# Optimization experiments

Measured on AMD Instinct MI355X. Metric: run time of the kernel, lower is better.

## Reference

```python
import jax, jax.numpy as jnp
import numpy as np

ATTEN_DIM = 64

def setup_inputs() -> dict:
    key = jax.random.key(0)
    ks = jax.random.split(key, 7)
    b, c, h, w = 16, 2048, 32, 32
    d_att, d_emb = 64, 64
    x = jax.random.normal(ks[0], (b, c, h, w), dtype=jnp.float32)
    # 1x1 conv == per-position linear; store weights as [out, in]
    scale = 1.0 / np.sqrt(c)
    wq = jax.random.normal(ks[1], (d_att, c), dtype=jnp.float32) * scale
    wk = jax.random.normal(ks[2], (d_att, c), dtype=jnp.float32) * scale
    wv = jax.random.normal(ks[3], (d_emb, c), dtype=jnp.float32) * scale
    bq = jnp.zeros((d_att,), dtype=jnp.float32)
    bk = jnp.zeros((d_att,), dtype=jnp.float32)
    bv = jnp.zeros((d_emb,), dtype=jnp.float32)
    return {"x": x, "wq": wq, "bq": bq, "wk": wk, "bk": bk, "wv": wv, "bv": bv}


def reference(x, wq, bq, wk, bk, wv, bv):
    b, c, h, w = x.shape
    # 1x1 conv projections: [b,c,h,w] x [d,c] -> [b,d,h,w]
    q = jnp.einsum('bchw,dc->bdhw', x, wq) + bq[None, :, None, None]
    k = jnp.einsum('bchw,dc->bdhw', x, wk) + bk[None, :, None, None]
    v = jnp.einsum('bchw,dc->bdhw', x, wv) + bv[None, :, None, None]
    # full non-local attention scores [b, h, w, h, w]
    atten = jnp.einsum('bcxy,bcij->bxyij', q, k) / ATTEN_DIM  # NOTE: module divides by atten_dim, not sqrt
    atten = jax.nn.softmax(atten.reshape(b, h, w, h * w), axis=-1).reshape(b, h, w, h, w)
    out = jnp.einsum('bxyij,bdij->bxyd', atten, v)
    return jnp.transpose(out, (0, 3, 1, 2))  # [b, emb_dim, h, w]
```

## Files before the change

### kernel.cpp

```cpp
#include <hip/hip_runtime.h>

typedef float f32x4 __attribute__((ext_vector_type(4)));
typedef short s16x8 __attribute__((ext_vector_type(8)));
typedef unsigned u32x4 __attribute__((ext_vector_type(4)));
typedef unsigned short u16;
typedef unsigned short u16x8 __attribute__((ext_vector_type(8)));

__device__ __forceinline__ u16 f2bf(float f) {
  unsigned u = __builtin_bit_cast(unsigned, f);
  u += 0x7fffu + ((u >> 16) & 1u);
  return (u16)(u >> 16);
}

__device__ __forceinline__ unsigned cvt_pk_bf16(float a, float b) {
  unsigned r;
  asm("v_cvt_pk_bf16_f32 %0, %1, %2" : "=v"(r) : "v"(a), "v"(b));
  return r;
}

#define AS1 __attribute__((address_space(1)))
#define AS3 __attribute__((address_space(3)))
#define GLD16(g, l) __builtin_amdgcn_global_load_lds((const AS1 unsigned int*)(g), (AS3 unsigned int*)(l), 16, 0, 0)

#define CEXP 0.0225421101f

__global__ __launch_bounds__(256) void prepack_w(
    const float* __restrict__ wq, const float* __restrict__ wk, const float* __restrict__ wv,
    u16* __restrict__ Wpk)
{
  const int d = blockIdx.x;
  const int t = threadIdx.x;
  const int kc = t >> 3, blk = t & 7;
  const int key = (d >> 1) & 7;
  const float* src = (d < 64) ? (wq + (size_t)d * 2048)
                   : (d < 128) ? (wk + (size_t)(d - 64) * 2048)
                               : (wv + (size_t)(d - 128) * 2048);
  const float* s8 = src + kc * 64 + ((blk ^ key) << 3);
  u16x8 o;
#pragma unroll
  for (int j = 0; j < 8; ++j) o[j] = f2bf(s8[j]);
  *(u16x8*)(Wpk + ((size_t)(kc * 192 + d) << 6) + (blk << 3)) = o;
}

__global__ __launch_bounds__(512) void qkv_proj(
    const float* __restrict__ x, const u16* __restrict__ Wpk,
    const float* __restrict__ bq, const float* __restrict__ bk, const float* __restrict__ bv,
    u16* __restrict__ Qo, u16* __restrict__ Ko, u16* __restrict__ Vt)
{
  const int b   = blockIdx.x >> 4;
  const int p0  = (blockIdx.x & 15) * 64;
  const int tid = threadIdx.x;
  const int lane = tid & 63;
  const int wid  = tid >> 6;
  const int l15 = lane & 15, l4 = lane >> 4;
  const int wm = wid & 1, wn = wid >> 1;

  __shared__ __align__(16) u16 lA[4][64 * 64];
  __shared__ __align__(16) u16 lB[4][192 * 64];

  const int pg = lane & 15;
  const int kb = wid * 4 + (lane >> 4);
  const int k0 = kb * 4;
  const int ww = wid - 4;

  f32x4 acc[2][3];
#pragma unroll
  for (int m = 0; m < 2; ++m)
#pragma unroll
    for (int n = 0; n < 3; ++n) acc[m][n] = (f32x4)(0.0f);

  const float* xb = x + (size_t)b * 2048 * 1024 + p0 + pg * 4;
  float4 SA[8], SB[8];

  auto xload2 = [&](int c, float4 (&S)[8]) {
#pragma unroll
    for (int cc = 0; cc < 2; ++cc) {
      const float* g = xb + (size_t)((c + cc) * 64 + k0) * 1024;
#pragma unroll
      for (int r = 0; r < 4; ++r) S[cc * 4 + r] = *(const float4*)(g + r * 1024);
    }
  };
  auto xstore2 = [&](int c, float4 (&S)[8]) {
#pragma unroll
    for (int cc = 0; cc < 2; ++cc) {
      const int slot = (c + cc) & 3;
#pragma unroll
      for (int col = 0; col < 4; ++col) {
        int p = pg * 4 + col;
        unsigned lo = cvt_pk_bf16(S[cc * 4 + 0][col], S[cc * 4 + 1][col]);
        unsigned hi = cvt_pk_bf16(S[cc * 4 + 2][col], S[cc * 4 + 3][col]);
        int swz = ((kb >> 1) ^ ((p >> 1) & 7)) & 7;
        char* dst = (char*)&lA[0][0] + slot * 8192 + p * 128 + (swz << 4) + (kb & 1) * 8;
        *(uint2*)dst = make_uint2(lo, hi);
      }
    }
  };
  auto wissue2 = [&](int c) {
#pragma unroll
    for (int cc = 0; cc < 2; ++cc) {
      const int slot = (c + cc) & 3;
      const u16* g = Wpk + (size_t)(c + cc) * 12288 + lane * 8;
#pragma unroll
      for (int j = 0; j < 6; ++j) {
        int q = ww * 6 + j;
        GLD16(g + q * 512, &lB[0][0] + slot * 12288 + q * 512);
      }
    }
  };
  auto domfma = [&](int slot) {
#pragma unroll
    for (int ks = 0; ks < 2; ++ks) {
      s16x8 af[2], bfv[3];
#pragma unroll
      for (int m = 0; m < 2; ++m) {
        int p = wm * 32 + m * 16 + l15;
        int swz = ((ks * 4 + l4) ^ ((p >> 1) & 7)) & 7;
        af[m] = *(const s16x8*)((const char*)&lA[0][0] + slot * 8192 + p * 128 + (swz << 4));
      }
#pragma unroll
      for (int n = 0; n < 3; ++n) {
        int d = wn * 48 + n * 16 + l15;
        int swz = ((ks * 4 + l4) ^ ((d >> 1) & 7)) & 7;
        bfv[n] = *(const s16x8*)((const char*)&lB[0][0] + slot * 24576 + d * 128 + (swz << 4));
      }
#pragma unroll
      for (int m = 0; m < 2; ++m)
#pragma unroll
        for (int n = 0; n < 3; ++n)
          acc[m][n] = __builtin_amdgcn_mfma_f32_16x16x32_bf16(af[m], bfv[n], acc[m][n], 0, 0, 0);
    }
  };
  auto barrier = [&]() {
    if (wid < 4) asm volatile("s_waitcnt lgkmcnt(0)" ::: "memory");
    else         asm volatile("s_waitcnt vmcnt(0) lgkmcnt(0)" ::: "memory");
    __builtin_amdgcn_sched_barrier(0);
    __builtin_amdgcn_s_barrier();
    __builtin_amdgcn_sched_barrier(0);
  };
  auto step = [&](int t, float4 (&Sl)[8], float4 (&Ss)[8]) {
    if (wid < 4) { if (t < 14) xload2(2 * t + 4, Sl); }
    else         { if (t < 15) wissue2(2 * t + 2); }
    __builtin_amdgcn_s_setprio(1);
    domfma((2 * t) & 3);
    domfma((2 * t + 1) & 3);
    __builtin_amdgcn_s_setprio(0);
    if (wid < 4 && t < 15) xstore2(2 * t + 2, Ss);
    barrier();
  };

  if (wid < 4) { xload2(0, SA); xload2(2, SB); xstore2(0, SA); }
  else         { wissue2(0); }
  barrier();

  for (int tt = 0; tt < 8; ++tt) {
    step(2 * tt,     SA, SB);
    step(2 * tt + 1, SB, SA);
  }

#pragma unroll
  for (int n = 0; n < 3; ++n) {
    const int dg = wn * 48 + n * 16 + l15;
    const int wi = dg >> 6, dl = dg & 63;
    const float* bsrc = (wi == 0) ? bq : (wi == 1) ? bk : bv;
    const float bias = bsrc[dl];
#pragma unroll
    for (int m = 0; m < 2; ++m) {
      const int pl = wm * 32 + m * 16 + l4 * 4;
      f32x4 a = acc[m][n];
      if (wi == 0) {
        u16* dst = Qo + ((size_t)b * 1024 + p0 + pl) * 64 + dl;
#pragma unroll
        for (int r = 0; r < 4; ++r) dst[(size_t)r * 64] = f2bf((a[r] + bias) * CEXP);
      } else if (wi == 1) {
#pragma unroll
        for (int r = 0; r < 4; ++r) {
          const int p = p0 + pl + r;
          const int p2 = (p & ~28) | ((p & 8) >> 1) | ((p & 16) >> 1) | ((p & 4) << 2);
          Ko[((size_t)b * 1024 + p2) * 64 + (((dl >> 3) ^ ((p2 >> 1) & 7)) << 3) + (dl & 7)]
            = f2bf(a[r] + bias);
        }
      } else {
        const int pk0 = p0 + pl;
        ushort4 hh;
        hh.x = f2bf(a[0] + bias); hh.y = f2bf(a[1] + bias);
        hh.z = f2bf(a[2] + bias); hh.w = f2bf(a[3] + bias);
        u16* dst = Vt + ((size_t)b * 64 + dl) * 1024 + (pk0 & ~127)
                 + (((((pk0 >> 3) & 15) ^ ((dl & 7) << 1)) & 15) << 3) + (pk0 & 7);
        *(ushort4*)dst = hh;
      }
    }
  }
}

__global__ __launch_bounds__(512) void attn_kernel(
    const u16* __restrict__ Qg, const u16* __restrict__ Kg,
    const u16* __restrict__ Vg, float* __restrict__ out)
{
  const int bid = blockIdx.x;
  const int b  = bid >> 4;
  const int qt = bid & 15;
  const int q0 = qt * 64;
  const int tid = threadIdx.x;
  const int lane = tid & 63;
  const int wid = tid >> 6;
  const int h = wid >> 2;
  const int w = wid & 3;
  const int l15 = lane & 15, l4 = lane >> 4;

  __shared__ __align__(16) char smem[131072];
  char* const gbase = smem + h * 65536;

  s16x8 qa[2];
#pragma unroll
  for (int ks = 0; ks < 2; ++ks)
    qa[ks] = *(const s16x8*)(Qg + ((size_t)b * 1024 + q0 + w * 16 + l15) * 64
                             + ks * 32 + l4 * 8);

  const u16* Kb = Kg + (size_t)b * 65536;
  const u16* Vb = Vg + (size_t)b * 65536;

  float l_run = 0.f;
  f32x4 oacc[4];
#pragma unroll
  for (int n = 0; n < 4; ++n) oacc[n] = (f32x4)(0.0f);

  auto kv_issue = [&](int tile, int buf) {
    const int pk0 = tile * 128;
#pragma unroll
    for (int jj = 0; jj < 4; ++jj)
      GLD16(Kb + (size_t)(pk0 + w * 32 + jj * 8) * 64 + lane * 8,
            gbase + buf * 16384 + (w * 4 + jj) * 1024);
#pragma unroll
    for (int jj = 0; jj < 4; ++jj)
      GLD16(Vb + (size_t)(w * 16 + jj * 4 + (lane >> 4)) * 1024 + pk0 + (lane & 15) * 8,
            gbase + 32768 + buf * 16384 + (w * 4 + jj) * 1024);
  };

  auto compute = [&](int buf) {
    const u16* kB = (const u16*)(gbase + buf * 16384);
    const u16* vB = (const u16*)(gbase + 32768 + buf * 16384);
    f32x4 sacc[8];
#pragma unroll
    for (int n = 0; n < 8; ++n) sacc[n] = (f32x4)(0.0f);
    __builtin_amdgcn_s_setprio(1);
#pragma unroll
    for (int ks = 0; ks < 2; ++ks) {
#pragma unroll
      for (int n = 0; n < 8; ++n) {
        int row = n * 16 + l15;
        s16x8 kv = *(const s16x8*)(kB + row * 64 +
                     (((ks * 4 + l4) ^ ((row >> 1) & 7)) << 3));
        sacc[n] = __builtin_amdgcn_mfma_f32_16x16x32_bf16(kv, qa[ks], sacc[n], 0, 0, 0);
      }
    }
    __builtin_amdgcn_s_setprio(0);

    unsigned c[8][2];
    float psum = 0.f;
#pragma unroll
    for (int n = 0; n < 8; ++n) {
      float e0 = exp2f(sacc[n][0]);
      float e1 = exp2f(sacc[n][1]);
      float e2 = exp2f(sacc[n][2]);
      float e3 = exp2f(sacc[n][3]);
      psum += (e0 + e1) + (e2 + e3);
      c[n][0] = cvt_pk_bf16(e0, e1);
      c[n][1] = cvt_pk_bf16(e2, e3);
    }
    psum += __shfl_xor(psum, 16);
    psum += __shfl_xor(psum, 32);
    l_run += psum;

    __builtin_amdgcn_s_setprio(1);
#pragma unroll
    for (int ks = 0; ks < 4; ++ks) {
      u32x4 t;
      t[0] = c[2 * ks][0];
      t[1] = c[2 * ks][1];
      t[2] = c[2 * ks + 1][0];
      t[3] = c[2 * ks + 1][1];
      s16x8 pfr = __builtin_bit_cast(s16x8, t);
#pragma unroll
      for (int n = 0; n < 4; ++n) {
        int row = n * 16 + l15;
        s16x8 vv = *(const s16x8*)(vB + row * 128 +
                     (((ks * 4 + l4) ^ ((row & 7) << 1)) << 3));
        oacc[n] = __builtin_amdgcn_mfma_f32_16x16x32_bf16(pfr, vv, oacc[n], 0, 0, 0);
      }
    }
    __builtin_amdgcn_s_setprio(0);
  };

  const int t0 = h * 4;
  kv_issue(t0, 0);
  kv_issue(t0 + 1, 1);
  asm volatile("s_waitcnt vmcnt(8)" ::: "memory");
  __builtin_amdgcn_sched_barrier(0);
  __builtin_amdgcn_s_barrier();
  __builtin_amdgcn_sched_barrier(0);

  for (int ic = 0; ic < 4; ++ic) {
    compute(ic & 1);
    if (ic < 3) {
      __builtin_amdgcn_sched_barrier(0);
      __builtin_amdgcn_s_barrier();
      __builtin_amdgcn_sched_barrier(0);
      if (ic + 2 < 4) {
        kv_issue(t0 + ic + 2, ic & 1);
        asm volatile("s_waitcnt vmcnt(8)" ::: "memory");
      } else {
        asm volatile("s_waitcnt vmcnt(0)" ::: "memory");
      }
      __builtin_amdgcn_sched_barrier(0);
      __builtin_amdgcn_s_barrier();
      __builtin_amdgcn_sched_barrier(0);
    }
  }

  float lr[4];
#pragma unroll
  for (int r = 0; r < 4; ++r) lr[r] = __shfl(l_run, l4 * 4 + r);

  __syncthreads();
  if (h == 1) {
    float* mrg = (float*)smem + (tid - 256) * 20;
#pragma unroll
    for (int n = 0; n < 4; ++n) *(f32x4*)(mrg + n * 4) = oacc[n];
#pragma unroll
    for (int r = 0; r < 4; ++r) mrg[16 + r] = lr[r];
  }
  __syncthreads();
  if (h == 0) {
    const float* mrg = (const float*)smem + tid * 20;
    float lt[4];
#pragma unroll
    for (int r = 0; r < 4; ++r) lt[r] = lr[r] + mrg[16 + r];
#pragma unroll
    for (int n = 0; n < 4; ++n) {
      f32x4 o1 = *(const f32x4*)(mrg + n * 4);
      float4 o;
      o.x = (oacc[n][0] + o1[0]) / lt[0];
      o.y = (oacc[n][1] + o1[1]) / lt[1];
      o.z = (oacc[n][2] + o1[2]) / lt[2];
      o.w = (oacc[n][3] + o1[3]) / lt[3];
      *(float4*)(out + ((size_t)b * 64 + n * 16 + l15) * 1024 + q0 + w * 16 + l4 * 4) = o;
    }
  }
}

extern "C" void kernel_launch(void* const* d_in, const int* in_sizes, int n_in,
                              void* d_out, int out_size, void* d_ws, size_t ws_size,
                              hipStream_t stream) {
  const float* x  = (const float*)d_in[0];
  const float* wq = (const float*)d_in[1];
  const float* bq = (const float*)d_in[2];
  const float* wk = (const float*)d_in[3];
  const float* bk = (const float*)d_in[4];
  const float* wv = (const float*)d_in[5];
  const float* bv = (const float*)d_in[6];
  float* out = (float*)d_out;

  u16* Qo  = (u16*)d_ws;
  u16* Ko  = Qo + (size_t)16 * 1024 * 64;
  u16* Vt  = Ko + (size_t)16 * 1024 * 64;
  u16* Wpk = Vt + (size_t)16 * 1024 * 64;

  prepack_w<<<192, 256, 0, stream>>>(wq, wk, wv, Wpk);
  qkv_proj<<<256, 512, 0, stream>>>(x, Wpk, bq, bk, bv, Qo, Ko, Vt);
  attn_kernel<<<256, 512, 0, stream>>>(Qo, Ko, Vt, out);
}
```

Before: 53.20 us.

## Split QKV projection output dims across two blocks to double grid size

Each qkv_proj block now computes half of the 192 output channels (96) for its 64 positions, so the grid doubles from 256 to 512 blocks and the LDS weight buffer halves. Per-wave work drops to one M-tile by three N-tiles. This gives more parallelism across the CUs and better occupancy, but every x tile is now loaded and converted to bf16 twice, doubling x read traffic for a kernel that is likely bandwidth-bound.

```diff
diff --git a/kernel.cpp b/kernel.cpp
--- a/kernel.cpp
+++ b/kernel.cpp
@@ -42,32 +42,32 @@
   *(u16x8*)(Wpk + ((size_t)(kc * 192 + d) << 6) + (blk << 3)) = o;
 }
 
-__global__ __launch_bounds__(512) void qkv_proj(
+__global__ __launch_bounds__(512, 4) void qkv_proj(
     const float* __restrict__ x, const u16* __restrict__ Wpk,
     const float* __restrict__ bq, const float* __restrict__ bk, const float* __restrict__ bv,
     u16* __restrict__ Qo, u16* __restrict__ Ko, u16* __restrict__ Vt)
 {
-  const int b   = blockIdx.x >> 4;
-  const int p0  = (blockIdx.x & 15) * 64;
+  const int b   = blockIdx.x >> 5;
+  const int p0  = ((blockIdx.x >> 1) & 15) * 64;
+  const int h   = blockIdx.x & 1;
   const int tid = threadIdx.x;
   const int lane = tid & 63;
   const int wid  = tid >> 6;
   const int l15 = lane & 15, l4 = lane >> 4;
-  const int wm = wid & 1, wn = wid >> 1;
+  const int wm = wid & 3;
+  const int wn = wid >> 2;
 
   __shared__ __align__(16) u16 lA[4][64 * 64];
-  __shared__ __align__(16) u16 lB[4][192 * 64];
+  __shared__ __align__(16) u16 lB[4][96 * 64];
 
   const int pg = lane & 15;
   const int kb = wid * 4 + (lane >> 4);
   const int k0 = kb * 4;
   const int ww = wid - 4;
 
-  f32x4 acc[2][3];
-#pragma unroll
-  for (int m = 0; m < 2; ++m)
-#pragma unroll
-    for (int n = 0; n < 3; ++n) acc[m][n] = (f32x4)(0.0f);
+  f32x4 acc[3];
+#pragma unroll
+  for (int n = 0; n < 3; ++n) acc[n] = (f32x4)(0.0f);
 
   const float* xb = x + (size_t)b * 2048 * 1024 + p0 + pg * 4;
   float4 SA[8], SB[8];
@@ -99,35 +99,27 @@
 #pragma unroll
     for (int cc = 0; cc < 2; ++cc) {
       const int slot = (c + cc) & 3;
-      const u16* g = Wpk + (size_t)(c + cc) * 12288 + lane * 8;
-#pragma unroll
-      for (int j = 0; j < 6; ++j) {
-        int q = ww * 6 + j;
-        GLD16(g + q * 512, &lB[0][0] + slot * 12288 + q * 512);
+      const u16* g = Wpk + (size_t)(c + cc) * 12288 + h * 6144 + lane * 8;
+#pragma unroll
+      for (int j = 0; j < 3; ++j) {
+        int q = ww * 3 + j;
+        GLD16(g + q * 512, (char*)&lB[0][0] + slot * 12288 + q * 1024);
       }
     }
   };
   auto domfma = [&](int slot) {
 #pragma unroll
     for (int ks = 0; ks < 2; ++ks) {
-      s16x8 af[2], bfv[3];
-#pragma unroll
-      for (int m = 0; m < 2; ++m) {
-        int p = wm * 32 + m * 16 + l15;
-        int swz = ((ks * 4 + l4) ^ ((p >> 1) & 7)) & 7;
-        af[m] = *(const s16x8*)((const char*)&lA[0][0] + slot * 8192 + p * 128 + (swz << 4));
-      }
+      const int p = wm * 16 + l15;
+      s16x8 af = *(const s16x8*)((const char*)&lA[0][0] + slot * 8192 + p * 128 +
+                   ((((ks * 4 + l4) ^ ((p >> 1) & 7)) & 7) << 4));
 #pragma unroll
       for (int n = 0; n < 3; ++n) {
-        int d = wn * 48 + n * 16 + l15;
-        int swz = ((ks * 4 + l4) ^ ((d >> 1) & 7)) & 7;
-        bfv[n] = *(const s16x8*)((const char*)&lB[0][0] + slot * 24576 + d * 128 + (swz << 4));
-      }
-#pragma unroll
-      for (int m = 0; m < 2; ++m)
-#pragma unroll
-        for (int n = 0; n < 3; ++n)
-          acc[m][n] = __builtin_amdgcn_mfma_f32_16x16x32_bf16(af[m], bfv[n], acc[m][n], 0, 0, 0);
+        const int dl = wn * 48 + n * 16 + l15;
+        s16x8 bv_ = *(const s16x8*)((const char*)&lB[0][0] + slot * 12288 + dl * 128 +
+                      ((((ks * 4 + l4) ^ ((dl >> 1) & 7)) & 7) << 4));
+        acc[n] = __builtin_amdgcn_mfma_f32_16x16x32_bf16(af, bv_, acc[n], 0, 0, 0);
+      }
     }
   };
   auto barrier = [&]() {
@@ -159,35 +151,32 @@
 
 #pragma unroll
   for (int n = 0; n < 3; ++n) {
-    const int dg = wn * 48 + n * 16 + l15;
+    const int dg = h * 96 + wn * 48 + n * 16 + l15;
     const int wi = dg >> 6, dl = dg & 63;
     const float* bsrc = (wi == 0) ? bq : (wi == 1) ? bk : bv;
     const float bias = bsrc[dl];
-#pragma unroll
-    for (int m = 0; m < 2; ++m) {
-      const int pl = wm * 32 + m * 16 + l4 * 4;
-      f32x4 a = acc[m][n];
-      if (wi == 0) {
-        u16* dst = Qo + ((size_t)b * 1024 + p0 + pl) * 64 + dl;
-#pragma unroll
-        for (int r = 0; r < 4; ++r) dst[(size_t)r * 64] = f2bf((a[r] + bias) * CEXP);
-      } else if (wi == 1) {
-#pragma unroll
-        for (int r = 0; r < 4; ++r) {
-          const int p = p0 + pl + r;
-          const int p2 = (p & ~28) | ((p & 8) >> 1) | ((p & 16) >> 1) | ((p & 4) << 2);
-          Ko[((size_t)b * 1024 + p2) * 64 + (((dl >> 3) ^ ((p2 >> 1) & 7)) << 3) + (dl & 7)]
-            = f2bf(a[r] + bias);
-        }
-      } else {
-        const int pk0 = p0 + pl;
-        ushort4 hh;
-        hh.x = f2bf(a[0] + bias); hh.y = f2bf(a[1] + bias);
-        hh.z = f2bf(a[2] + bias); hh.w = f2bf(a[3] + bias);
-        u16* dst = Vt + ((size_t)b * 64 + dl) * 1024 + (pk0 & ~127)
-                 + (((((pk0 >> 3) & 15) ^ ((dl & 7) << 1)) & 15) << 3) + (pk0 & 7);
-        *(ushort4*)dst = hh;
-      }
+    const int pl = wm * 16 + l4 * 4;
+    f32x4 a = acc[n];
+    if (wi == 0) {
+      u16* dst = Qo + ((size_t)b * 1024 + p0 + pl) * 64 + dl;
+#pragma unroll
+      for (int r = 0; r < 4; ++r) dst[(size_t)r * 64] = f2bf((a[r] + bias) * CEXP);
+    } else if (wi == 1) {
+#pragma unroll
+      for (int r = 0; r < 4; ++r) {
+        const int p = p0 + pl + r;
+        const int p2 = (p & ~28) | ((p & 8) >> 1) | ((p & 16) >> 1) | ((p & 4) << 2);
+        Ko[((size_t)b * 1024 + p2) * 64 + (((dl >> 3) ^ ((p2 >> 1) & 7)) << 3) + (dl & 7)]
+          = f2bf(a[r] + bias);
+      }
+    } else {
+      const int pk0 = p0 + pl;
+      ushort4 hh;
+      hh.x = f2bf(a[0] + bias); hh.y = f2bf(a[1] + bias);
+      hh.z = f2bf(a[2] + bias); hh.w = f2bf(a[3] + bias);
+      u16* dst = Vt + ((size_t)b * 64 + dl) * 1024 + (pk0 & ~127)
+               + (((((pk0 >> 3) & 15) ^ ((dl & 7) << 1)) & 15) << 3) + (pk0 & 7);
+      *(ushort4*)dst = hh;
     }
   }
 }
@@ -366,6 +355,6 @@
   u16* Wpk = Vt + (size_t)16 * 1024 * 64;
 
   prepack_w<<<192, 256, 0, stream>>>(wq, wk, wv, Wpk);
-  qkv_proj<<<256, 512, 0, stream>>>(x, Wpk, bq, bk, bv, Qo, Ko, Vt);
+  qkv_proj<<<512, 512, 0, stream>>>(x, Wpk, bq, bk, bv, Qo, Ko, Vt);
   attn_kernel<<<256, 512, 0, stream>>>(Qo, Ko, Vt, out);
 }
```

Result: slower. 69.75 us (+31.1%).

## Load projection weights directly into registers and split x staging across all waves

Applied to the files above, without the earlier changes.

The QKV projection kernel no longer stages the packed weights through LDS with global_load_lds. Each wave now loads its B fragments straight from global memory into registers, double-buffered across iterations, and the weight prepack drops its XOR swizzle to match the new direct layout. All eight waves now share the x-to-bf16 staging (half the channels per wave group) instead of four producer waves doing it alone. This frees most of the LDS and removes the weight ds_reads. In exchange it raises VGPR pressure (24 s16x8 weight registers) and sends redundant per-wave global weight reads through L2.

```diff
diff --git a/kernel.cpp b/kernel.cpp
--- a/kernel.cpp
+++ b/kernel.cpp
@@ -31,11 +31,10 @@
   const int d = blockIdx.x;
   const int t = threadIdx.x;
   const int kc = t >> 3, blk = t & 7;
-  const int key = (d >> 1) & 7;
   const float* src = (d < 64) ? (wq + (size_t)d * 2048)
                    : (d < 128) ? (wk + (size_t)(d - 64) * 2048)
                                : (wv + (size_t)(d - 128) * 2048);
-  const float* s8 = src + kc * 64 + ((blk ^ key) << 3);
+  const float* s8 = src + kc * 64 + (blk << 3);
   u16x8 o;
 #pragma unroll
   for (int j = 0; j < 8; ++j) o[j] = f2bf(s8[j]);
@@ -54,14 +53,13 @@
   const int wid  = tid >> 6;
   const int l15 = lane & 15, l4 = lane >> 4;
   const int wm = wid & 1, wn = wid >> 1;
+  const int g  = wid >> 2;
 
   __shared__ __align__(16) u16 lA[4][64 * 64];
-  __shared__ __align__(16) u16 lB[4][192 * 64];
 
   const int pg = lane & 15;
-  const int kb = wid * 4 + (lane >> 4);
+  const int kb = (wid & 3) * 4 + (lane >> 4);
   const int k0 = kb * 4;
-  const int ww = wid - 4;
 
   f32x4 acc[2][3];
 #pragma unroll
@@ -70,47 +68,39 @@
     for (int n = 0; n < 3; ++n) acc[m][n] = (f32x4)(0.0f);
 
   const float* xb = x + (size_t)b * 2048 * 1024 + p0 + pg * 4;
-  float4 SA[8], SB[8];
-
-  auto xload2 = [&](int c, float4 (&S)[8]) {
-#pragma unroll
-    for (int cc = 0; cc < 2; ++cc) {
-      const float* g = xb + (size_t)((c + cc) * 64 + k0) * 1024;
-#pragma unroll
-      for (int r = 0; r < 4; ++r) S[cc * 4 + r] = *(const float4*)(g + r * 1024);
-    }
-  };
-  auto xstore2 = [&](int c, float4 (&S)[8]) {
-#pragma unroll
-    for (int cc = 0; cc < 2; ++cc) {
-      const int slot = (c + cc) & 3;
-#pragma unroll
-      for (int col = 0; col < 4; ++col) {
-        int p = pg * 4 + col;
-        unsigned lo = cvt_pk_bf16(S[cc * 4 + 0][col], S[cc * 4 + 1][col]);
-        unsigned hi = cvt_pk_bf16(S[cc * 4 + 2][col], S[cc * 4 + 3][col]);
-        int swz = ((kb >> 1) ^ ((p >> 1) & 7)) & 7;
-        char* dst = (char*)&lA[0][0] + slot * 8192 + p * 128 + (swz << 4) + (kb & 1) * 8;
-        *(uint2*)dst = make_uint2(lo, hi);
-      }
-    }
-  };
-  auto wissue2 = [&](int c) {
-#pragma unroll
-    for (int cc = 0; cc < 2; ++cc) {
-      const int slot = (c + cc) & 3;
-      const u16* g = Wpk + (size_t)(c + cc) * 12288 + lane * 8;
-#pragma unroll
-      for (int j = 0; j < 6; ++j) {
-        int q = ww * 6 + j;
-        GLD16(g + q * 512, &lB[0][0] + slot * 12288 + q * 512);
-      }
-    }
-  };
-  auto domfma = [&](int slot) {
+  const u16* wb = Wpk + ((size_t)wn * 48 + l15) * 64 + l4 * 8;
+  float4 Sa[4], Sb[4];
+  s16x8 WA[6], WB[6], WC[6], WD[6];
+
+  auto xload1 = [&](int c, float4 (&S)[4]) {
+    const float* gp = xb + (size_t)(c * 64 + k0) * 1024;
+#pragma unroll
+    for (int r = 0; r < 4; ++r) S[r] = *(const float4*)(gp + r * 1024);
+  };
+  auto xstore1 = [&](int c, float4 (&S)[4]) {
+    const int slot = c & 3;
+#pragma unroll
+    for (int col = 0; col < 4; ++col) {
+      int p = pg * 4 + col;
+      unsigned lo = cvt_pk_bf16(S[0][col], S[1][col]);
+      unsigned hi = cvt_pk_bf16(S[2][col], S[3][col]);
+      int swz = ((kb >> 1) ^ ((p >> 1) & 7)) & 7;
+      char* dst = (char*)&lA[0][0] + slot * 8192 + p * 128 + (swz << 4) + (kb & 1) * 8;
+      *(uint2*)dst = make_uint2(lo, hi);
+    }
+  };
+  auto wload = [&](int c, s16x8 (&W)[6]) {
+    const u16* gp = wb + (size_t)c * 12288;
+#pragma unroll
+    for (int ks = 0; ks < 2; ++ks)
+#pragma unroll
+      for (int n = 0; n < 3; ++n)
+        W[ks * 3 + n] = *(const s16x8*)(gp + n * 1024 + ks * 32);
+  };
+  auto domfma = [&](int slot, s16x8 (&W)[6]) {
 #pragma unroll
     for (int ks = 0; ks < 2; ++ks) {
-      s16x8 af[2], bfv[3];
+      s16x8 af[2];
 #pragma unroll
       for (int m = 0; m < 2; ++m) {
         int p = wm * 32 + m * 16 + l15;
@@ -118,43 +108,49 @@
         af[m] = *(const s16x8*)((const char*)&lA[0][0] + slot * 8192 + p * 128 + (swz << 4));
       }
 #pragma unroll
-      for (int n = 0; n < 3; ++n) {
-        int d = wn * 48 + n * 16 + l15;
-        int swz = ((ks * 4 + l4) ^ ((d >> 1) & 7)) & 7;
-        bfv[n] = *(const s16x8*)((const char*)&lB[0][0] + slot * 24576 + d * 128 + (swz << 4));
-      }
-#pragma unroll
       for (int m = 0; m < 2; ++m)
 #pragma unroll
         for (int n = 0; n < 3; ++n)
-          acc[m][n] = __builtin_amdgcn_mfma_f32_16x16x32_bf16(af[m], bfv[n], acc[m][n], 0, 0, 0);
+          acc[m][n] = __builtin_amdgcn_mfma_f32_16x16x32_bf16(af[m], W[ks * 3 + n], acc[m][n], 0, 0, 0);
     }
   };
   auto barrier = [&]() {
-    if (wid < 4) asm volatile("s_waitcnt lgkmcnt(0)" ::: "memory");
-    else         asm volatile("s_waitcnt vmcnt(0) lgkmcnt(0)" ::: "memory");
+    asm volatile("s_waitcnt lgkmcnt(0)" ::: "memory");
     __builtin_amdgcn_sched_barrier(0);
     __builtin_amdgcn_s_barrier();
     __builtin_amdgcn_sched_barrier(0);
   };
-  auto step = [&](int t, float4 (&Sl)[8], float4 (&Ss)[8]) {
-    if (wid < 4) { if (t < 14) xload2(2 * t + 4, Sl); }
-    else         { if (t < 15) wissue2(2 * t + 2); }
-    __builtin_amdgcn_s_setprio(1);
-    domfma((2 * t) & 3);
-    domfma((2 * t + 1) & 3);
-    __builtin_amdgcn_s_setprio(0);
-    if (wid < 4 && t < 15) xstore2(2 * t + 2, Ss);
-    barrier();
-  };
-
-  if (wid < 4) { xload2(0, SA); xload2(2, SB); xstore2(0, SA); }
-  else         { wissue2(0); }
+
+  xload1(g, Sa);
+  xload1(2 + g, Sb);
+  wload(0, WA);
+  wload(1, WB);
+  xstore1(g, Sa);
   barrier();
 
   for (int tt = 0; tt < 8; ++tt) {
-    step(2 * tt,     SA, SB);
-    step(2 * tt + 1, SB, SA);
+    {
+      const int t0 = 2 * tt;
+      if (t0 + 1 < 16) { wload(2 * t0 + 2, WC); wload(2 * t0 + 3, WD); }
+      if (t0 < 14) xload1(2 * t0 + 4 + g, Sa);
+      __builtin_amdgcn_s_setprio(1);
+      domfma((2 * t0) & 3, WA);
+      domfma((2 * t0 + 1) & 3, WB);
+      __builtin_amdgcn_s_setprio(0);
+      if (t0 < 15) xstore1(2 * t0 + 2 + g, Sb);
+      barrier();
+    }
+    {
+      const int t1 = 2 * tt + 1;
+      if (t1 + 1 < 16) { wload(2 * t1 + 2, WA); wload(2 * t1 + 3, WB); }
+      if (t1 < 14) xload1(2 * t1 + 4 + g, Sb);
+      __builtin_amdgcn_s_setprio(1);
+      domfma((2 * t1) & 3, WC);
+      domfma((2 * t1 + 1) & 3, WD);
+      __builtin_amdgcn_s_setprio(0);
+      if (t1 < 15) xstore1(2 * t1 + 2 + g, Sa);
+      barrier();
+    }
   }
 
 #pragma unroll
```

New measurement: 73.34 us. +37.9%, slower.
